# Kernel optimization log

Hardware: AMD Instinct MI355X
Metric: run time of the kernel (lower is better)

## Reference

```python
import jax, jax.numpy as jnp
import numpy as np

CHUNK = 32
PRIOR = 64
POSE = 512
PRED = 128
B = 2048


def setup_inputs() -> dict:
    key = jax.random.key(0)
    k1, k2, k3, k4, k5, k6 = jax.random.split(key, 6)
    initial_feature = jax.random.normal(k1, (B, PRIOR, POSE), dtype=jnp.float32)
    pred_feature = jax.random.normal(k2, (B, PRED, POSE), dtype=jnp.float32)
    s1 = 1.0 / np.sqrt(CHUNK * POSE)
    s2 = 1.0 / np.sqrt(POSE)
    W1 = jax.random.uniform(k3, (POSE, CHUNK * POSE), minval=-s1, maxval=s1, dtype=jnp.float32)
    b1 = jax.random.uniform(k4, (POSE,), minval=-s1, maxval=s1, dtype=jnp.float32)
    W2 = jax.random.uniform(k5, (POSE, POSE), minval=-s2, maxval=s2, dtype=jnp.float32)
    b2 = jax.random.uniform(k6, (POSE,), minval=-s2, maxval=s2, dtype=jnp.float32)
    return {"initial_feature": initial_feature, "pred_feature": pred_feature,
            "W1": W1, "b1": b1, "W2": W2, "b2": b2}


def reference(initial_feature, pred_feature, W1, b1, W2, b2):
    Bn = initial_feature.shape[0]
    # last CHUNK prior frames flattened -> [B, CHUNK*POSE]
    x = initial_feature[:, PRIOR - CHUNK:, :].reshape(Bn, -1)
    # spatial_chunk_encoder (Dropout is identity in eval mode)
    mem = (x @ W1.T + b1) @ W2.T + b2          # [B, POSE]
    head = pred_feature[:, :CHUNK, :]          # [B, CHUNK, POSE]
    score = jnp.einsum('bd,bcd->bc', mem, head)  # per-token dot product
    g = jax.nn.sigmoid(score)[..., None]       # [B, CHUNK, 1]
    blended = g * head + (1.0 - g) * mem[:, None, :]
    return pred_feature.at[:, :CHUNK, :].set(blended)
```

## Files before the change

### kernel.cpp

```cpp
#include <hip/hip_runtime.h>
#include <hip/hip_bf16.h>
#include <stdint.h>

#define CHUNKC 32
#define PRIORC 64
#define POSEC 512
#define PREDC 128
#define NB 2048
#define K1 (CHUNKC*POSEC)
#define KS 8
#define KCH (K1/KS)

typedef __attribute__((ext_vector_type(8))) short bf16x8;
typedef __attribute__((ext_vector_type(4))) float f32x4;

__device__ __forceinline__ unsigned short f2b(float f) {
    union { float f; unsigned int u; } x; x.f = f;
    unsigned int r = x.u + 0x7fffu + ((x.u >> 16) & 1u);
    return (unsigned short)(r >> 16);
}

__device__ __forceinline__ void gload_lds16(const void* g, void* l) {
    __builtin_amdgcn_global_load_lds(
        (const __attribute__((address_space(1))) unsigned int*)g,
        (__attribute__((address_space(3))) unsigned int*)l, 16, 0, 0);
}


__global__ __launch_bounds__(256) void cvt_x_kernel(const float4* __restrict__ src,
                                                    ushort4* __restrict__ dst) {
    const int64_t n = (int64_t)NB * 4096;
    const int64_t stride = (int64_t)gridDim.x * blockDim.x;
    for (int64_t i = (int64_t)blockIdx.x * blockDim.x + threadIdx.x; i < n; i += stride) {
        int64_t b = i >> 12, r = i & 4095;
        float4 v = src[b * 8192 + 4096 + r];
        dst[i] = make_ushort4(f2b(v.x), f2b(v.y), f2b(v.z), f2b(v.w));
    }
}

__global__ __launch_bounds__(256) void cvt_flat_kernel(const float4* __restrict__ src,
                                                       ushort4* __restrict__ dst, int64_t n4) {
    const int64_t stride = (int64_t)gridDim.x * blockDim.x;
    for (int64_t i = (int64_t)blockIdx.x * blockDim.x + threadIdx.x; i < n4; i += stride) {
        float4 v = src[i];
        dst[i] = make_ushort4(f2b(v.x), f2b(v.y), f2b(v.z), f2b(v.w));
    }
}

__global__ __launch_bounds__(256) void gemm1_kernel(const ushort* __restrict__ xb,
                                                    const ushort* __restrict__ w1b,
                                                    float* __restrict__ part) {
    __shared__ ushort As[128][64];
    __shared__ ushort Bs[128][64];
    const int t = threadIdx.x;
    const int l = t & 63, wid = t >> 6;
    const int wr = wid >> 1, wc = wid & 1;
    const int bid = blockIdx.x;
    const int mt = bid & 15, nt = (bid >> 4) & 3, ks = bid >> 6;

    f32x4 acc[4][4] = {};

    const ushort* aG = xb  + (int64_t)(mt * 128) * K1 + ks * KCH;
    const ushort* bG = w1b + (int64_t)(nt * 128) * K1 + ks * KCH;
    const int srow = t >> 3, scol = (t & 7) * 8;

    const int fr = l & 15, fq = l >> 4;

    for (int k0 = 0; k0 < KCH; k0 += 64) {
#pragma unroll
        for (int i = 0; i < 4; ++i) {
            gload_lds16(aG + (int64_t)(i * 32 + srow) * K1 + k0 + scol,
                        (char*)&As[0][0] + i * 4096 + wid * 1024);
            gload_lds16(bG + (int64_t)(i * 32 + srow) * K1 + k0 + scol,
                        (char*)&Bs[0][0] + i * 4096 + wid * 1024);
        }
        __syncthreads();
#pragma unroll
        for (int k2 = 0; k2 < 2; ++k2) {
            bf16x8 a[4], b[4];
#pragma unroll
            for (int m = 0; m < 4; ++m)
                a[m] = *(const bf16x8*)&As[wr * 64 + m * 16 + fr][k2 * 32 + fq * 8];
#pragma unroll
            for (int n = 0; n < 4; ++n)
                b[n] = *(const bf16x8*)&Bs[wc * 64 + n * 16 + fr][k2 * 32 + fq * 8];
#pragma unroll
            for (int m = 0; m < 4; ++m)
#pragma unroll
                for (int n = 0; n < 4; ++n)
                    acc[m][n] = __builtin_amdgcn_mfma_f32_16x16x32_bf16(a[m], b[n], acc[m][n], 0, 0, 0);
        }
        __syncthreads();
    }

    float* P = part + (int64_t)ks * NB * POSEC;
    const int mbase = mt * 128 + wr * 64, nbase = nt * 128 + wc * 64;
#pragma unroll
    for (int m = 0; m < 4; ++m)
#pragma unroll
        for (int n = 0; n < 4; ++n) {
            int row0 = mbase + m * 16 + fq * 4;
            int col  = nbase + n * 16 + fr;
#pragma unroll
            for (int r = 0; r < 4; ++r)
                P[(int64_t)(row0 + r) * POSEC + col] = acc[m][n][r];
        }
}

__global__ __launch_bounds__(256) void reduce_kernel(const float4* __restrict__ part,
                                                     const float* __restrict__ b1,
                                                     ushort4* __restrict__ A2) {
    const int i4 = blockIdx.x * 256 + threadIdx.x;
    float4 s = part[i4];
#pragma unroll
    for (int k = 1; k < KS; ++k) {
        float4 p = part[(int64_t)k * 262144 + i4];
        s.x += p.x; s.y += p.y; s.z += p.z; s.w += p.w;
    }
    const int col = (i4 * 4) & 511;
    float4 bv = *(const float4*)&b1[col];
    A2[i4] = make_ushort4(f2b(s.x + bv.x), f2b(s.y + bv.y), f2b(s.z + bv.z), f2b(s.w + bv.w));
}

__global__ __launch_bounds__(256) void gemm2_kernel(const ushort* __restrict__ A2,
                                                    const ushort* __restrict__ w2b,
                                                    const float* __restrict__ b2,
                                                    float* __restrict__ mem) {
    __shared__ ushort As[64][64];
    __shared__ ushort Bs[64][64];
    const int t = threadIdx.x;
    const int l = t & 63, wid = t >> 6;
    const int wr = wid >> 1, wc = wid & 1;
    const int mt = blockIdx.x >> 3, nt = blockIdx.x & 7;

    f32x4 acc[2][2] = {};
    const ushort* aG = A2  + (int64_t)(mt * 64) * POSEC;
    const ushort* bG = w2b + (int64_t)(nt * 64) * POSEC;
    const int srow = t >> 3, scol = (t & 7) * 8;
    const int fr = l & 15, fq = l >> 4;

    for (int k0 = 0; k0 < POSEC; k0 += 64) {
#pragma unroll
        for (int i = 0; i < 2; ++i) {
            gload_lds16(aG + (int64_t)(i * 32 + srow) * POSEC + k0 + scol,
                        (char*)&As[0][0] + i * 4096 + wid * 1024);
            gload_lds16(bG + (int64_t)(i * 32 + srow) * POSEC + k0 + scol,
                        (char*)&Bs[0][0] + i * 4096 + wid * 1024);
        }
        __syncthreads();
#pragma unroll
        for (int k2 = 0; k2 < 2; ++k2) {
            bf16x8 a[2], b[2];
#pragma unroll
            for (int m = 0; m < 2; ++m)
                a[m] = *(const bf16x8*)&As[wr * 32 + m * 16 + fr][k2 * 32 + fq * 8];
#pragma unroll
            for (int n = 0; n < 2; ++n)
                b[n] = *(const bf16x8*)&Bs[wc * 32 + n * 16 + fr][k2 * 32 + fq * 8];
#pragma unroll
            for (int m = 0; m < 2; ++m)
#pragma unroll
                for (int n = 0; n < 2; ++n)
                    acc[m][n] = __builtin_amdgcn_mfma_f32_16x16x32_bf16(a[m], b[n], acc[m][n], 0, 0, 0);
        }
        __syncthreads();
    }

    const int mbase = mt * 64 + wr * 32, nbase = nt * 64 + wc * 32;
#pragma unroll
    for (int m = 0; m < 2; ++m)
#pragma unroll
        for (int n = 0; n < 2; ++n) {
            int row0 = mbase + m * 16 + fq * 4;
            int col  = nbase + n * 16 + fr;
            float bias = b2[col];
#pragma unroll
            for (int r = 0; r < 4; ++r)
                mem[(int64_t)(row0 + r) * POSEC + col] = acc[m][n][r] + bias;
        }
}

__global__ __launch_bounds__(256) void blend_kernel(const float* __restrict__ pred,
                                                    const float* __restrict__ mem,
                                                    float* __restrict__ out) {
    const int b = blockIdx.x;
    const int t = threadIdx.x;
    __shared__ float sm[POSEC];
    __shared__ float sg[CHUNKC];

    sm[t]       = mem[(int64_t)b * POSEC + t];
    sm[t + 256] = mem[(int64_t)b * POSEC + 256 + t];
    __syncthreads();

    const int l = t & 63, wid = t >> 6;
    const float4* sm4 = (const float4*)sm;
    const float4* p4 = (const float4*)pred + (int64_t)b * 16384;
    float4* o4 = (float4*)out + (int64_t)b * 16384;

#pragma unroll
    for (int ci = 0; ci < 8; ++ci) {
        int c = wid * 8 + ci;
        float4 h0 = p4[c * 128 + l * 2];
        float4 h1 = p4[c * 128 + l * 2 + 1];
        float4 m0 = sm4[l * 2];
        float4 m1 = sm4[l * 2 + 1];
        float s = h0.x * m0.x + h0.y * m0.y + h0.z * m0.z + h0.w * m0.w
                + h1.x * m1.x + h1.y * m1.y + h1.z * m1.z + h1.w * m1.w;
#pragma unroll
        for (int o = 32; o; o >>= 1) s += __shfl_xor(s, o);
        if (l == 0) sg[c] = 1.0f / (1.0f + expf(-s));
    }
    __syncthreads();

#pragma unroll
    for (int i = 0; i < 16; ++i) {
        int idx = i * 256 + t;
        int row = idx >> 7, c4 = idx & 127;
        float g = sg[row];
        float4 h = p4[idx];
        float4 m = sm4[c4];
        float4 r;
        r.x = g * h.x + (1.0f - g) * m.x;
        r.y = g * h.y + (1.0f - g) * m.y;
        r.z = g * h.z + (1.0f - g) * m.z;
        r.w = g * h.w + (1.0f - g) * m.w;
        o4[idx] = r;
    }
#pragma unroll
    for (int i = 0; i < 48; ++i) {
        int idx = 4096 + i * 256 + t;
        o4[idx] = p4[idx];
    }
}


extern "C" void kernel_launch(void* const* d_in, const int* in_sizes, int n_in,
                              void* d_out, int out_size, void* d_ws, size_t ws_size,
                              hipStream_t stream) {
    const float* init = (const float*)d_in[0];
    const float* pred = (const float*)d_in[1];
    const float* W1   = (const float*)d_in[2];
    const float* b1   = (const float*)d_in[3];
    const float* W2   = (const float*)d_in[4];
    const float* b2   = (const float*)d_in[5];
    float* out = (float*)d_out;

    char* ws = (char*)d_ws;
    ushort* xb   = (ushort*)(ws);
    ushort* w1b  = (ushort*)(ws + 67108864);
    ushort* w2b  = (ushort*)(ws + 83886080);
    float*  part = (float*) (ws + 84410368);
    ushort* A2   = (ushort*)(ws + 117964800);
    float*  mem  = (float*) (ws + 120061952);

    cvt_x_kernel<<<2048, 256, 0, stream>>>((const float4*)init, (ushort4*)xb);
    cvt_flat_kernel<<<1024, 256, 0, stream>>>((const float4*)W1, (ushort4*)w1b,
                                              (int64_t)POSEC * K1 / 4);
    cvt_flat_kernel<<<256, 256, 0, stream>>>((const float4*)W2, (ushort4*)w2b,
                                             (int64_t)POSEC * POSEC / 4);
    gemm1_kernel<<<512, 256, 0, stream>>>(xb, w1b, part);
    reduce_kernel<<<1024, 256, 0, stream>>>((const float4*)part, b1, (ushort4*)A2);
    gemm2_kernel<<<256, 256, 0, stream>>>(A2, w2b, b2, mem);
    blend_kernel<<<NB, 256, 0, stream>>>(pred, mem, out);
}
```

Measured before the change: 335.8 us.

## Merge conversion kernels and overlap tail copy with GEMM1 blocks

Folds the three fp32-to-bf16 conversion kernels into one launch. It also moves the copy of the untouched pred_feature rows (frames 32..127) out of the blend kernel and into extra blocks appended to the GEMM1 grid. The bandwidth-bound copy can then run alongside the compute-bound GEMM blocks instead of sitting on the critical path at the end. The cost is a branch per element in the conversion loop and copy blocks competing with GEMM blocks for CU slots and memory bandwidth.

```diff
diff --git a/kernel.cpp b/kernel.cpp
--- a/kernel.cpp
+++ b/kernel.cpp
@@ -26,36 +26,58 @@
         (__attribute__((address_space(3))) unsigned int*)l, 16, 0, 0);
 }
 
-
-__global__ __launch_bounds__(256) void cvt_x_kernel(const float4* __restrict__ src,
-                                                    ushort4* __restrict__ dst) {
-    const int64_t n = (int64_t)NB * 4096;
+#define XN4   8388608
+#define W1N4  2097152
+#define W2N4  65536
+__global__ __launch_bounds__(256) void cvt_all_kernel(const float4* __restrict__ init,
+                                                      const float4* __restrict__ W1,
+                                                      const float4* __restrict__ W2,
+                                                      ushort4* __restrict__ xb,
+                                                      ushort4* __restrict__ w1b,
+                                                      ushort4* __restrict__ w2b) {
+    const int64_t n = XN4 + W1N4 + W2N4;
     const int64_t stride = (int64_t)gridDim.x * blockDim.x;
     for (int64_t i = (int64_t)blockIdx.x * blockDim.x + threadIdx.x; i < n; i += stride) {
-        int64_t b = i >> 12, r = i & 4095;
-        float4 v = src[b * 8192 + 4096 + r];
-        dst[i] = make_ushort4(f2b(v.x), f2b(v.y), f2b(v.z), f2b(v.w));
-    }
-}
-
-__global__ __launch_bounds__(256) void cvt_flat_kernel(const float4* __restrict__ src,
-                                                       ushort4* __restrict__ dst, int64_t n4) {
-    const int64_t stride = (int64_t)gridDim.x * blockDim.x;
-    for (int64_t i = (int64_t)blockIdx.x * blockDim.x + threadIdx.x; i < n4; i += stride) {
-        float4 v = src[i];
-        dst[i] = make_ushort4(f2b(v.x), f2b(v.y), f2b(v.z), f2b(v.w));
-    }
-}
-
-__global__ __launch_bounds__(256) void gemm1_kernel(const ushort* __restrict__ xb,
-                                                    const ushort* __restrict__ w1b,
-                                                    float* __restrict__ part) {
+        float4 v; ushort4* dst;
+        if (i < XN4) {
+            int64_t b = i >> 12, r = i & 4095;
+            v = init[b * 8192 + 4096 + r];
+            dst = xb + i;
+        } else if (i < XN4 + W1N4) {
+            v = W1[i - XN4];
+            dst = w1b + (i - XN4);
+        } else {
+            v = W2[i - XN4 - W1N4];
+            dst = w2b + (i - XN4 - W1N4);
+        }
+        *dst = make_ushort4(f2b(v.x), f2b(v.y), f2b(v.z), f2b(v.w));
+    }
+}
+
+__global__ __launch_bounds__(256) void gemm1_copy_kernel(const ushort* __restrict__ xb,
+                                                         const ushort* __restrict__ w1b,
+                                                         float* __restrict__ part,
+                                                         const float4* __restrict__ pred4,
+                                                         float4* __restrict__ out4) {
     __shared__ ushort As[128][64];
     __shared__ ushort Bs[128][64];
     const int t = threadIdx.x;
+    const int bid = blockIdx.x;
+
+    if (bid >= 512) {
+        const int cid = bid - 512;
+        const int b = cid >> 1, h = cid & 1;
+        const int64_t base = (int64_t)b * 16384 + 4096 + h * 6144;
+#pragma unroll
+        for (int i = 0; i < 24; ++i) {
+            int64_t idx = base + i * 256 + t;
+            out4[idx] = pred4[idx];
+        }
+        return;
+    }
+
     const int l = t & 63, wid = t >> 6;
     const int wr = wid >> 1, wc = wid & 1;
-    const int bid = blockIdx.x;
     const int mt = bid & 15, nt = (bid >> 4) & 3, ks = bid >> 6;
 
     f32x4 acc[4][4] = {};
@@ -180,9 +202,9 @@
         }
 }
 
-__global__ __launch_bounds__(256) void blend_kernel(const float* __restrict__ pred,
-                                                    const float* __restrict__ mem,
-                                                    float* __restrict__ out) {
+__global__ __launch_bounds__(256) void blend_head_kernel(const float* __restrict__ pred,
+                                                         const float* __restrict__ mem,
+                                                         float* __restrict__ out) {
     const int b = blockIdx.x;
     const int t = threadIdx.x;
     __shared__ float sm[POSEC];
@@ -226,11 +248,6 @@
         r.w = g * h.w + (1.0f - g) * m.w;
         o4[idx] = r;
     }
-#pragma unroll
-    for (int i = 0; i < 48; ++i) {
-        int idx = 4096 + i * 256 + t;
-        o4[idx] = p4[idx];
-    }
 }
 
 
@@ -253,13 +270,12 @@
     ushort* A2   = (ushort*)(ws + 117964800);
     float*  mem  = (float*) (ws + 120061952);
 
-    cvt_x_kernel<<<2048, 256, 0, stream>>>((const float4*)init, (ushort4*)xb);
-    cvt_flat_kernel<<<1024, 256, 0, stream>>>((const float4*)W1, (ushort4*)w1b,
-                                              (int64_t)POSEC * K1 / 4);
-    cvt_flat_kernel<<<256, 256, 0, stream>>>((const float4*)W2, (ushort4*)w2b,
-                                             (int64_t)POSEC * POSEC / 4);
-    gemm1_kernel<<<512, 256, 0, stream>>>(xb, w1b, part);
+    cvt_all_kernel<<<2560, 256, 0, stream>>>((const float4*)init, (const float4*)W1,
+                                             (const float4*)W2,
+                                             (ushort4*)xb, (ushort4*)w1b, (ushort4*)w2b);
+    gemm1_copy_kernel<<<512 + 4096, 256, 0, stream>>>(xb, w1b, part,
+                                                      (const float4*)pred, (float4*)out);
     reduce_kernel<<<1024, 256, 0, stream>>>((const float4*)part, b1, (ushort4*)A2);
     gemm2_kernel<<<256, 256, 0, stream>>>(A2, w2b, b2, mem);
-    blend_kernel<<<NB, 256, 0, stream>>>(pred, mem, out);
-}
+    blend_head_kernel<<<NB, 256, 0, stream>>>(pred, mem, out);
+}
```

After: 352.9 us. 5.1% more time.

## Fuse activation bf16 conversion into GEMM1 loads, merge weight casts, double split-K

Applied to the files above, without the earlier changes.

GEMM1 now reads the fp32 activations straight from the input and converts them to bf16 in registers before writing LDS. This removes the separate activation conversion pass and its 64MB bf16 scratch round trip. The W1 and W2 conversions are merged into one launch, and split-K goes from 8 to 16, doubling GEMM1's grid to 1024 blocks. The cost is that activation loads become synchronous register loads instead of async LDS loads, and the partial-sum buffer and the reduce work both double.

```diff
diff --git a/kernel.cpp b/kernel.cpp
--- a/kernel.cpp
+++ b/kernel.cpp
@@ -8,10 +8,11 @@
 #define PREDC 128
 #define NB 2048
 #define K1 (CHUNKC*POSEC)
-#define KS 8
+#define KS 16
 #define KCH (K1/KS)
 
 typedef __attribute__((ext_vector_type(8))) short bf16x8;
+typedef __attribute__((ext_vector_type(8))) unsigned short u16x8;
 typedef __attribute__((ext_vector_type(4))) float f32x4;
 
 __device__ __forceinline__ unsigned short f2b(float f) {
@@ -26,28 +27,23 @@
         (__attribute__((address_space(3))) unsigned int*)l, 16, 0, 0);
 }
 
-
-__global__ __launch_bounds__(256) void cvt_x_kernel(const float4* __restrict__ src,
-                                                    ushort4* __restrict__ dst) {
-    const int64_t n = (int64_t)NB * 4096;
+#define W1N4  2097152
+#define W2N4  65536
+__global__ __launch_bounds__(256) void cvt_w_kernel(const float4* __restrict__ W1,
+                                                    const float4* __restrict__ W2,
+                                                    ushort4* __restrict__ w1b,
+                                                    ushort4* __restrict__ w2b) {
+    const int64_t n = W1N4 + W2N4;
     const int64_t stride = (int64_t)gridDim.x * blockDim.x;
     for (int64_t i = (int64_t)blockIdx.x * blockDim.x + threadIdx.x; i < n; i += stride) {
-        int64_t b = i >> 12, r = i & 4095;
-        float4 v = src[b * 8192 + 4096 + r];
-        dst[i] = make_ushort4(f2b(v.x), f2b(v.y), f2b(v.z), f2b(v.w));
-    }
-}
-
-__global__ __launch_bounds__(256) void cvt_flat_kernel(const float4* __restrict__ src,
-                                                       ushort4* __restrict__ dst, int64_t n4) {
-    const int64_t stride = (int64_t)gridDim.x * blockDim.x;
-    for (int64_t i = (int64_t)blockIdx.x * blockDim.x + threadIdx.x; i < n4; i += stride) {
-        float4 v = src[i];
-        dst[i] = make_ushort4(f2b(v.x), f2b(v.y), f2b(v.z), f2b(v.w));
-    }
-}
-
-__global__ __launch_bounds__(256) void gemm1_kernel(const ushort* __restrict__ xb,
+        float4 v; ushort4* dst;
+        if (i < W1N4) { v = W1[i]; dst = w1b + i; }
+        else          { v = W2[i - W1N4]; dst = w2b + (i - W1N4); }
+        *dst = make_ushort4(f2b(v.x), f2b(v.y), f2b(v.z), f2b(v.w));
+    }
+}
+
+__global__ __launch_bounds__(256) void gemm1_kernel(const float* __restrict__ init,
                                                     const ushort* __restrict__ w1b,
                                                     float* __restrict__ part) {
     __shared__ ushort As[128][64];
@@ -60,19 +56,28 @@
 
     f32x4 acc[4][4] = {};
 
-    const ushort* aG = xb  + (int64_t)(mt * 128) * K1 + ks * KCH;
+    const float* aG = init + (int64_t)(mt * 128) * 32768 + 16384 + ks * KCH;
     const ushort* bG = w1b + (int64_t)(nt * 128) * K1 + ks * KCH;
     const int srow = t >> 3, scol = (t & 7) * 8;
+    const int arow = t >> 3, akc = (t & 7) * 8;
 
     const int fr = l & 15, fq = l >> 4;
 
     for (int k0 = 0; k0 < KCH; k0 += 64) {
 #pragma unroll
-        for (int i = 0; i < 4; ++i) {
-            gload_lds16(aG + (int64_t)(i * 32 + srow) * K1 + k0 + scol,
-                        (char*)&As[0][0] + i * 4096 + wid * 1024);
+        for (int i = 0; i < 4; ++i)
             gload_lds16(bG + (int64_t)(i * 32 + srow) * K1 + k0 + scol,
                         (char*)&Bs[0][0] + i * 4096 + wid * 1024);
+#pragma unroll
+        for (int i = 0; i < 4; ++i) {
+            int row = i * 32 + arow;
+            const float* src = aG + (int64_t)row * 32768 + k0 + akc;
+            float4 v0 = *(const float4*)(src);
+            float4 v1 = *(const float4*)(src + 4);
+            u16x8 w;
+            w[0] = f2b(v0.x); w[1] = f2b(v0.y); w[2] = f2b(v0.z); w[3] = f2b(v0.w);
+            w[4] = f2b(v1.x); w[5] = f2b(v1.y); w[6] = f2b(v1.z); w[7] = f2b(v1.w);
+            *(u16x8*)&As[row][akc] = w;
         }
         __syncthreads();
 #pragma unroll
@@ -246,19 +251,15 @@
     float* out = (float*)d_out;
 
     char* ws = (char*)d_ws;
-    ushort* xb   = (ushort*)(ws);
-    ushort* w1b  = (ushort*)(ws + 67108864);
-    ushort* w2b  = (ushort*)(ws + 83886080);
-    float*  part = (float*) (ws + 84410368);
-    ushort* A2   = (ushort*)(ws + 117964800);
-    float*  mem  = (float*) (ws + 120061952);
-
-    cvt_x_kernel<<<2048, 256, 0, stream>>>((const float4*)init, (ushort4*)xb);
-    cvt_flat_kernel<<<1024, 256, 0, stream>>>((const float4*)W1, (ushort4*)w1b,
-                                              (int64_t)POSEC * K1 / 4);
-    cvt_flat_kernel<<<256, 256, 0, stream>>>((const float4*)W2, (ushort4*)w2b,
-                                             (int64_t)POSEC * POSEC / 4);
-    gemm1_kernel<<<512, 256, 0, stream>>>(xb, w1b, part);
+    ushort* w1b  = (ushort*)(ws);
+    ushort* w2b  = (ushort*)(ws + 16777216);
+    float*  part = (float*) (ws + 17301504);
+    ushort* A2   = (ushort*)(ws + 84410368);
+    float*  mem  = (float*) (ws + 86507520);
+
+    cvt_w_kernel<<<1024, 256, 0, stream>>>((const float4*)W1, (const float4*)W2,
+                                           (ushort4*)w1b, (ushort4*)w2b);
+    gemm1_kernel<<<1024, 256, 0, stream>>>(init, w1b, part);
     reduce_kernel<<<1024, 256, 0, stream>>>((const float4*)part, b1, (ushort4*)A2);
     gemm2_kernel<<<256, 256, 0, stream>>>(A2, w2b, b2, mem);
     blend_kernel<<<NB, 256, 0, stream>>>(pred, mem, out);
```

Measured after the change: 340.8 us. About the same (+1.5%).
